# Optimization experiments

Measured on AMD Instinct MI355X. Metric: run time of the kernel, lower is better.

## Reference

```python
import jax, jax.numpy as jnp
import numpy as np

NEG = -1e9

def setup_inputs() -> dict:
    key = jax.random.key(0)
    k1, k2, k3 = jax.random.split(key, 3)
    b, t, d = 16, 2048, 64
    q = jax.random.normal(k1, (b, t, d), dtype=jnp.float32)
    k = jax.random.normal(k2, (b, t, d), dtype=jnp.float32)
    v = jax.random.normal(k3, (b, t, d), dtype=jnp.float32)
    return {"q": q, "k": k, "v": v}

def reference(q, k, v):
    # q:[b,tq,d], k:[b,tk,d], v:[b,tk,dv]
    dim_k = k.shape[-1]
    t_q, t_k = q.shape[1], k.shape[1]
    qk = jnp.einsum('bqd,bkd->bqk', q, k) / jnp.sqrt(jnp.float32(dim_k))
    # causal mask: positions j > i are masked (triu with diag offset 1)
    causal = jnp.triu(jnp.ones((t_q, t_k), dtype=bool), k=1)  # [tq,tk]
    qk = jnp.where(causal[None, :, :], NEG, qk)
    sm_qk = jax.nn.softmax(qk, axis=-1)
    out = jnp.einsum('bqk,bkd->bqd', sm_qk, v)
    return (out, sm_qk)
```

## Files before the change

### kernel.cpp

```cpp
#include <hip/hip_runtime.h>
#include <hip/hip_bf16.h>


#define BATCHES 16
#define SEQ 2048
#define DIM 64
#define QB 64
#define KT 64
#define KT1 128
#define NQB (SEQ / QB)
#define KLD 72
#define VLD 72
#define PFLD 68

#define BAR() do { asm volatile("s_waitcnt lgkmcnt(0)" ::: "memory"); \
                   __builtin_amdgcn_s_barrier(); } while (0)

typedef __attribute__((ext_vector_type(8))) short bf16x8;
typedef __attribute__((ext_vector_type(4))) short short4v;
typedef __attribute__((ext_vector_type(4))) float f32x4;

static __device__ __forceinline__ short f2bf(float f) {
    return __builtin_bit_cast(short, __float2bfloat16(f));
}
static __device__ __forceinline__ float bf2f(short s) {
    unsigned int u = ((unsigned int)(unsigned short)s) << 16;
    return __builtin_bit_cast(float, u);
}
static __device__ __forceinline__ void split8(f32x4 a, f32x4 b, float sc,
                                              bf16x8& hh, bf16x8& ll) {
#pragma unroll
    for (int e = 0; e < 4; ++e) {
        float x = a[e] * sc; short hb = f2bf(x);
        hh[e] = hb; ll[e] = f2bf(x - bf2f(hb));
    }
#pragma unroll
    for (int e = 0; e < 4; ++e) {
        float x = b[e] * sc; short hb = f2bf(x);
        hh[4 + e] = hb; ll[4 + e] = f2bf(x - bf2f(hb));
    }
}

#define SMEM_BYTES 81408

__global__ __launch_bounds__(512, 2) void sdpa_fused(
    const float* __restrict__ Qg, const float* __restrict__ Kg,
    const float* __restrict__ Vg, float* __restrict__ Og, float* __restrict__ Pg)
{
    const int i = blockIdx.x;
    const int g = i & 7;
    const int j = i >> 3;
    const int b = 2 * g + (j >> 5);
    const int jj = j & 31;
    const int qb = (j < 32) ? jj : (31 - jj);
    const int q0 = qb * QB;

    const int tid = threadIdx.x;
    const int lane = tid & 63;
    const int wave = tid >> 6;
    const int wr = wave & 3;
    const int h  = wave >> 2;
    const int lo = lane & 15;
    const int hi = lane >> 4;
    const bool kStager = (wave < 4);
    const int stid = kStager ? tid : (tid - 256);
    const int sr = stid >> 4;
    const int sc_ = (stid & 15) * 4;
    const int vr = (stid >> 4) * 4;
    const int s1r = tid >> 4;
    const int s1c = (tid & 15) * 4;

    __shared__ __align__(16) char smem[SMEM_BYTES];
    short (*Khi)[KT * KLD]  = reinterpret_cast<short (*)[KT * KLD]>(smem);
    short (*Vt)[DIM * VLD]  = reinterpret_cast<short (*)[DIM * VLD]>(smem + 18432);
    float (*Pf)[QB * PFLD]  = reinterpret_cast<float (*)[QB * PFLD]>(smem + 46080);
    float (*lS)[QB]         = reinterpret_cast<float (*)[QB]>(smem + 80896);
    short (*K1)[KT1 * KLD]  = reinterpret_cast<short (*)[KT1 * KLD]>(smem);

    const float* qB = Qg + (size_t)b * SEQ * DIM;
    const float* kB = Kg + (size_t)b * SEQ * DIM;
    const float* vB = Vg + (size_t)b * SEQ * DIM;

    bf16x8 qa0h, qa0l, qa1h, qa1l;
    {
        const float* qr = &qB[(size_t)(q0 + wr * 16 + lo) * DIM + hi * 8];
        split8(*(const f32x4*)qr,        *(const f32x4*)(qr + 4),  0.125f, qa0h, qa0l);
        split8(*(const f32x4*)(qr + 32), *(const f32x4*)(qr + 36), 0.125f, qa1h, qa1l);
    }

    const int nkt = qb + 1;

    const int r16z = tid >> 4;
    const int c4z = (tid & 15) * 4;
    float* zrow0 = &Pg[((size_t)(b * SEQ) + (NQB - 1 - qb) * QB + r16z) * SEQ + c4z];
    float* zrow1 = zrow0 + (size_t)32 * SEQ;

    float rl[4] = {0.f, 0.f, 0.f, 0.f};
    {
        const int nkt1 = (nkt + 1) >> 1;
        auto loadK1 = [&](f32x4* kp, int t) {
#pragma unroll
            for (int ii = 0; ii < 4; ++ii)
                kp[ii] = *(const f32x4*)&kB[(size_t)(t * KT1 + s1r + 32 * ii) * DIM + s1c];
        };
        auto stageK1 = [&](int buf, const f32x4* kp) {
#pragma unroll
            for (int ii = 0; ii < 4; ++ii) {
                short4v hh;
#pragma unroll
                for (int e = 0; e < 4; ++e) hh[e] = f2bf(kp[ii][e]);
                *(short4v*)&K1[buf][(s1r + 32 * ii) * KLD + s1c] = hh;
            }
        };
        f32x4 kp[4];
        loadK1(kp, 0);
        stageK1(0, kp);
        if (nkt1 > 1) loadK1(kp, 1);
        BAR();
        const int bandMax = q0 + wr * 16 + 15;
        for (int t = 0; t < nkt1; ++t) {
            const int cur = t & 1;
            if (t + 1 < nkt1) {
                stageK1(cur ^ 1, kp);
                if (t + 2 < nkt1) loadK1(kp, t + 2);
            }
            const int base = t * KT1;
#pragma unroll
            for (int nn = 0; nn < 4; ++nn) {
                const int n = 4 * h + nn;
                const int cbase = base + 16 * n;
                if (cbase > bandMax) continue;
                bf16x8 kh0 = *(const bf16x8*)&K1[cur][(16 * n + lo) * KLD + hi * 8];
                bf16x8 kh1 = *(const bf16x8*)&K1[cur][(16 * n + lo) * KLD + 32 + hi * 8];
                f32x4 acc = {0.f, 0.f, 0.f, 0.f};
                __builtin_amdgcn_s_setprio(1);
                acc = __builtin_amdgcn_mfma_f32_16x16x32_bf16(qa0h, kh0, acc, 0, 0, 0);
                acc = __builtin_amdgcn_mfma_f32_16x16x32_bf16(qa1h, kh1, acc, 0, 0, 0);
                __builtin_amdgcn_s_setprio(0);
                if (cbase + 15 <= q0 + wr * 16) {
#pragma unroll
                    for (int jx = 0; jx < 4; ++jx) rl[jx] += __expf(acc[jx]);
                } else {
                    const int col = cbase + lo;
#pragma unroll
                    for (int jx = 0; jx < 4; ++jx)
                        if (col <= q0 + wr * 16 + hi * 4 + jx) rl[jx] += __expf(acc[jx]);
                }
            }
            BAR();
        }
    }
#pragma unroll
    for (int m = 1; m <= 8; m <<= 1)
#pragma unroll
        for (int jx = 0; jx < 4; ++jx) rl[jx] += __shfl_xor(rl[jx], m, 16);
    if (lo == 0) {
#pragma unroll
        for (int jx = 0; jx < 4; ++jx)
            lS[h][wr * 16 + hi * 4 + jx] = rl[jx];
    }
    BAR();
    float il[4];
#pragma unroll
    for (int jx = 0; jx < 4; ++jx) {
        const int row = wr * 16 + hi * 4 + jx;
        il[jx] = 1.0f / (lS[0][row] + lS[1][row]);
    }
    BAR();

    const int n0 = 2 * h;
    f32x4 o2[2];
#pragma unroll
    for (int nn = 0; nn < 2; ++nn) { o2[nn][0] = 0.f; o2[nn][1] = 0.f; o2[nn][2] = 0.f; o2[nn][3] = 0.f; }

    auto loadK = [&](f32x4* kp, int kt) {
#pragma unroll
        for (int ii = 0; ii < 4; ++ii)
            kp[ii] = *(const f32x4*)&kB[(size_t)(kt * KT + sr + 16 * ii) * DIM + sc_];
    };
    auto loadV = [&](f32x4* vp, int kt) {
#pragma unroll
        for (int ii = 0; ii < 4; ++ii)
            vp[ii] = *(const f32x4*)&vB[(size_t)(kt * KT + vr + ii) * DIM + sc_];
    };
    auto stageKhi = [&](int buf, const f32x4* kp) {
#pragma unroll
        for (int ii = 0; ii < 4; ++ii) {
            short4v hh;
#pragma unroll
            for (int e = 0; e < 4; ++e) hh[e] = f2bf(kp[ii][e]);
            *(short4v*)&Khi[buf][(sr + 16 * ii) * KLD + sc_] = hh;
        }
    };
    auto stageVt = [&](int buf, const f32x4* vp) {
#pragma unroll
        for (int e = 0; e < 4; ++e) {
            short4v tv;
#pragma unroll
            for (int ii = 0; ii < 4; ++ii) tv[ii] = f2bf(vp[ii][e]);
            *(short4v*)&Vt[buf][(sc_ + e) * VLD + vr] = tv;
        }
    };
    auto rowStore = [&](int pbuf, int kt) {
        float* dstb = &Pg[((size_t)(b * SEQ) + q0 + wave * 8) * SEQ + kt * KT + lane];
#pragma unroll
        for (int rr = 0; rr < 8; ++rr)
            dstb[(size_t)rr * SEQ] = Pf[pbuf][(wave * 8 + rr) * PFLD + lane];
    };
    auto pvStep = [&](int pbuf, int vbuf) {
        const float* pr = &Pf[pbuf][(wr * 16 + lo) * PFLD + hi * 8];
        f32x4 a = *(const f32x4*)pr, c2 = *(const f32x4*)(pr + 4);
        f32x4 d = *(const f32x4*)(pr + 32), e2 = *(const f32x4*)(pr + 36);
        bf16x8 pa0, pa1;
#pragma unroll
        for (int e = 0; e < 4; ++e) {
            pa0[e] = f2bf(a[e]); pa0[4 + e] = f2bf(c2[e]);
            pa1[e] = f2bf(d[e]); pa1[4 + e] = f2bf(e2[e]);
        }
        __builtin_amdgcn_s_setprio(1);
#pragma unroll
        for (int nn = 0; nn < 2; ++nn) {
            const int n = n0 + nn;
            bf16x8 vb0 = *(const bf16x8*)&Vt[vbuf][(16 * n + lo) * VLD + hi * 8];
            bf16x8 vb1 = *(const bf16x8*)&Vt[vbuf][(16 * n + lo) * VLD + 32 + hi * 8];
            o2[nn] = __builtin_amdgcn_mfma_f32_16x16x32_bf16(pa0, vb0, o2[nn], 0, 0, 0);
            o2[nn] = __builtin_amdgcn_mfma_f32_16x16x32_bf16(pa1, vb1, o2[nn], 0, 0, 0);
        }
        __builtin_amdgcn_s_setprio(0);
    };

    {
        f32x4 kp[4], vp[4];
        if (kStager) {
            loadK(kp, 0); stageKhi(0, kp);
            if (nkt > 1) loadK(kp, 1);
        } else {
            loadV(vp, 0); stageVt(0, vp);
            if (nkt > 1) loadV(vp, 1);
        }
        BAR();

        int vstg = 1, vprev = 2;
        for (int kt = 0; kt < nkt; ++kt) {
            const int cur = kt & 1;
            const int pcur = kt & 1;
            if (kt < qb) {
                const int zt = (NQB - qb) + kt;
                const f32x4 zv = {0.f, 0.f, 0.f, 0.f};
                *(f32x4*)&zrow0[zt * KT] = zv;
                *(f32x4*)&zrow1[zt * KT] = zv;
            }
            if (kt + 1 < nkt) {
                if (kStager) {
                    stageKhi(cur ^ 1, kp);
                    if (kt + 2 < nkt) loadK(kp, kt + 2);
                } else {
                    stageVt(vstg, vp);
                    if (kt + 2 < nkt) loadV(vp, kt + 2);
                }
            }
            if (kt > 0) {
                rowStore(pcur ^ 1, kt - 1);
                pvStep(pcur ^ 1, vprev);
            }
#pragma unroll
            for (int nn = 0; nn < 2; ++nn) {
                const int n = n0 + nn;
                const bool fm = (kt == qb) && (n > wr);
                f32x4 acc = {0.f, 0.f, 0.f, 0.f};
                if (!fm) {
                    bf16x8 kh0 = *(const bf16x8*)&Khi[cur][(16 * n + lo) * KLD + hi * 8];
                    bf16x8 kh1 = *(const bf16x8*)&Khi[cur][(16 * n + lo) * KLD + 32 + hi * 8];
                    __builtin_amdgcn_s_setprio(1);
                    acc = __builtin_amdgcn_mfma_f32_16x16x32_bf16(qa0h, kh0, acc, 0, 0, 0);
                    acc = __builtin_amdgcn_mfma_f32_16x16x32_bf16(qa1h, kh1, acc, 0, 0, 0);
                    acc = __builtin_amdgcn_mfma_f32_16x16x32_bf16(qa0l, kh0, acc, 0, 0, 0);
                    acc = __builtin_amdgcn_mfma_f32_16x16x32_bf16(qa1l, kh1, acc, 0, 0, 0);
                    __builtin_amdgcn_s_setprio(0);
                }
                const int col = 16 * n + lo;
#pragma unroll
                for (int jx = 0; jx < 4; ++jx) {
                    const int row = wr * 16 + hi * 4 + jx;
                    const float p = (!fm && (kt < qb || col <= row)) ? __expf(acc[jx]) * il[jx] : 0.f;
                    Pf[pcur][row * PFLD + col] = p;
                }
            }
            BAR();
            vprev = (vprev == 2) ? 0 : vprev + 1;
            vstg  = (vstg  == 2) ? 0 : vstg  + 1;
        }
        {
            const int pl = (nkt - 1) & 1;
            const int vl = (nkt - 1) % 3;
            rowStore(pl, nkt - 1);
            pvStep(pl, vl);
        }
    }

    {
        float* og = &Og[((size_t)(b * SEQ) + q0 + wr * 16 + hi * 4) * DIM + lo];
#pragma unroll
        for (int jx = 0; jx < 4; ++jx)
#pragma unroll
            for (int nn = 0; nn < 2; ++nn)
                og[jx * DIM + (n0 + nn) * 16] = o2[nn][jx];
    }
}

extern "C" void kernel_launch(void* const* d_in, const int* in_sizes, int n_in,
                              void* d_out, int out_size, void* d_ws, size_t ws_size,
                              hipStream_t stream) {
    const float* q = (const float*)d_in[0];
    const float* k = (const float*)d_in[1];
    const float* v = (const float*)d_in[2];
    float* out  = (float*)d_out;
    float* smqk = out + (size_t)BATCHES * SEQ * DIM;

    sdpa_fused<<<NQB * BATCHES, 512, 0, stream>>>(q, k, v, out, smqk);
}
```

Before: 95.50 us.

## Store P tile as bf16 in single LDS buffer to cut shared memory and raise occupancy

The probability tile in LDS changes from double-buffered fp32 to a single bf16 buffer, and the V staging ring drops from triple to double buffering. This cuts static shared memory from about 81KB to about 46KB, and the launch bound asks for 6 blocks per SM instead of 2. The software pipeline that overlapped the previous tile's row store and PV step with the current QK step is replaced by a serialized QK, barrier, store/PV, barrier sequence. Side effects: the returned softmax matrix is now rounded through bf16, which loses precision, and the extra barrier per iteration removes overlap.

Measured after the change: 153.5 us. 1.61x slower.

```diff
diff --git a/kernel.cpp b/kernel.cpp
--- a/kernel.cpp
+++ b/kernel.cpp
@@ -11,7 +11,7 @@
 #define NQB (SEQ / QB)
 #define KLD 72
 #define VLD 72
-#define PFLD 68
+#define PBLD 72
 
 #define BAR() do { asm volatile("s_waitcnt lgkmcnt(0)" ::: "memory"); \
                    __builtin_amdgcn_s_barrier(); } while (0)
@@ -41,9 +41,9 @@
     }
 }
 
-#define SMEM_BYTES 81408
-
-__global__ __launch_bounds__(512, 2) void sdpa_fused(
+#define SMEM_BYTES 46592
+
+__global__ __launch_bounds__(512, 6) void sdpa_fused(
     const float* __restrict__ Qg, const float* __restrict__ Kg,
     const float* __restrict__ Vg, float* __restrict__ Og, float* __restrict__ Pg)
 {
@@ -73,8 +73,8 @@
     __shared__ __align__(16) char smem[SMEM_BYTES];
     short (*Khi)[KT * KLD]  = reinterpret_cast<short (*)[KT * KLD]>(smem);
     short (*Vt)[DIM * VLD]  = reinterpret_cast<short (*)[DIM * VLD]>(smem + 18432);
-    float (*Pf)[QB * PFLD]  = reinterpret_cast<float (*)[QB * PFLD]>(smem + 46080);
-    float (*lS)[QB]         = reinterpret_cast<float (*)[QB]>(smem + 80896);
+    short* Pb               = reinterpret_cast<short*>(smem + 36864);
+    float (*lS)[QB]         = reinterpret_cast<float (*)[QB]>(smem + 46080);
     short (*K1)[KT1 * KLD]  = reinterpret_cast<short (*)[KT1 * KLD]>(smem);
 
     const float* qB = Qg + (size_t)b * SEQ * DIM;
@@ -201,22 +201,15 @@
             *(short4v*)&Vt[buf][(sc_ + e) * VLD + vr] = tv;
         }
     };
-    auto rowStore = [&](int pbuf, int kt) {
+    auto rowStore = [&](int kt) {
         float* dstb = &Pg[((size_t)(b * SEQ) + q0 + wave * 8) * SEQ + kt * KT + lane];
 #pragma unroll
         for (int rr = 0; rr < 8; ++rr)
-            dstb[(size_t)rr * SEQ] = Pf[pbuf][(wave * 8 + rr) * PFLD + lane];
-    };
-    auto pvStep = [&](int pbuf, int vbuf) {
-        const float* pr = &Pf[pbuf][(wr * 16 + lo) * PFLD + hi * 8];
-        f32x4 a = *(const f32x4*)pr, c2 = *(const f32x4*)(pr + 4);
-        f32x4 d = *(const f32x4*)(pr + 32), e2 = *(const f32x4*)(pr + 36);
-        bf16x8 pa0, pa1;
-#pragma unroll
-        for (int e = 0; e < 4; ++e) {
-            pa0[e] = f2bf(a[e]); pa0[4 + e] = f2bf(c2[e]);
-            pa1[e] = f2bf(d[e]); pa1[4 + e] = f2bf(e2[e]);
-        }
+            dstb[(size_t)rr * SEQ] = bf2f(Pb[(wave * 8 + rr) * PBLD + lane]);
+    };
+    auto pvStep = [&](int vbuf) {
+        bf16x8 pa0 = *(const bf16x8*)&Pb[(wr * 16 + lo) * PBLD + hi * 8];
+        bf16x8 pa1 = *(const bf16x8*)&Pb[(wr * 16 + lo) * PBLD + 32 + hi * 8];
         __builtin_amdgcn_s_setprio(1);
 #pragma unroll
         for (int nn = 0; nn < 2; ++nn) {
@@ -240,10 +233,8 @@
         }
         BAR();
 
-        int vstg = 1, vprev = 2;
         for (int kt = 0; kt < nkt; ++kt) {
             const int cur = kt & 1;
-            const int pcur = kt & 1;
             if (kt < qb) {
                 const int zt = (NQB - qb) + kt;
                 const f32x4 zv = {0.f, 0.f, 0.f, 0.f};
@@ -255,13 +246,9 @@
                     stageKhi(cur ^ 1, kp);
                     if (kt + 2 < nkt) loadK(kp, kt + 2);
                 } else {
-                    stageVt(vstg, vp);
+                    stageVt(cur ^ 1, vp);
                     if (kt + 2 < nkt) loadV(vp, kt + 2);
                 }
-            }
-            if (kt > 0) {
-                rowStore(pcur ^ 1, kt - 1);
-                pvStep(pcur ^ 1, vprev);
             }
 #pragma unroll
             for (int nn = 0; nn < 2; ++nn) {
@@ -283,18 +270,13 @@
                 for (int jx = 0; jx < 4; ++jx) {
                     const int row = wr * 16 + hi * 4 + jx;
                     const float p = (!fm && (kt < qb || col <= row)) ? __expf(acc[jx]) * il[jx] : 0.f;
-                    Pf[pcur][row * PFLD + col] = p;
+                    Pb[row * PBLD + col] = f2bf(p);
                 }
             }
             BAR();
-            vprev = (vprev == 2) ? 0 : vprev + 1;
-            vstg  = (vstg  == 2) ? 0 : vstg  + 1;
-        }
-        {
-            const int pl = (nkt - 1) & 1;
-            const int vl = (nkt - 1) % 3;
-            rowStore(pl, nkt - 1);
-            pvStep(pl, vl);
+            rowStore(kt);
+            pvStep(cur);
+            BAR();
         }
     }
 
```
